# Optimization experiments

Measured on AMD Instinct MI355X. Metric: run time of the kernel, lower is better.

## Reference

```python
import jax, jax.numpy as jnp
import numpy as np

NUM_HEADS = 16
THETA = 10000.0


def _rope(x, cos, sin):
    # x: [B, H, S, d_k]; cos/sin: [S, d_k//2]
    x_even = x[..., 0::2]
    x_odd = x[..., 1::2]
    out_even = x_even * cos - x_odd * sin
    out_odd = x_odd * cos + x_even * sin
    # interleave back to original even/odd layout
    return jnp.stack([out_even, out_odd], axis=-1).reshape(x.shape)


def setup_inputs() -> dict:
    key = jax.random.key(0)
    ks = jax.random.split(key, 5)
    B, S, D = 2, 2048, 1024
    std = 2.0 / (D + D)
    return {
        "x": jax.random.normal(ks[0], (B, S, D), dtype=jnp.float32),
        "w_q": jax.random.normal(ks[1], (D, D), dtype=jnp.float32) * std,
        "w_k": jax.random.normal(ks[2], (D, D), dtype=jnp.float32) * std,
        "w_v": jax.random.normal(ks[3], (D, D), dtype=jnp.float32) * std,
        "w_o": jax.random.normal(ks[4], (D, D), dtype=jnp.float32) * std,
    }


def reference(x, w_q, w_k, w_v, w_o):
    B, S, D = x.shape
    H = NUM_HEADS
    d_k = D // H

    # QKV projections: x @ W.T
    q = jnp.einsum('bsd,ed->bse', x, w_q).reshape(B, S, H, d_k).transpose(0, 2, 1, 3)
    k = jnp.einsum('bsd,ed->bse', x, w_k).reshape(B, S, H, d_k).transpose(0, 2, 1, 3)
    v = jnp.einsum('bsd,ed->bse', x, w_v).reshape(B, S, H, d_k).transpose(0, 2, 1, 3)

    # RoPE (token_positions = arange(S))
    pos = jnp.arange(S, dtype=jnp.float32)
    inv_freq = 1.0 / (THETA ** (2.0 * jnp.arange(d_k // 2, dtype=jnp.float32) / d_k))
    angles = pos[:, None] * inv_freq[None, :]  # [S, d_k//2]
    cos, sin = jnp.cos(angles), jnp.sin(angles)
    q = _rope(q, cos, sin)
    k = _rope(k, cos, sin)

    # causal attention
    scores = jnp.einsum('bhqd,bhkd->bhqk', q, k) / jnp.sqrt(jnp.float32(d_k))
    causal = jnp.tril(jnp.ones((S, S), dtype=bool))
    scores = jnp.where(causal[None, None], scores, -jnp.inf)
    attn = jax.nn.softmax(scores, axis=-1)
    out = jnp.einsum('bhqk,bhkd->bhqd', attn, v)  # [B, H, S, d_k]

    out = out.transpose(0, 2, 1, 3).reshape(B, S, D)
    return jnp.einsum('bsd,ed->bse', out, w_o)
```

## Files before the change

### kernel.cpp

```cpp
#include <hip/hip_runtime.h>

typedef unsigned short u16;
typedef unsigned int u32;
typedef short bf16x8 __attribute__((ext_vector_type(8)));
typedef float f32x4 __attribute__((ext_vector_type(4)));

#define CSC 0.18033688011112042f

__device__ __forceinline__ u16 f2bf(float f) {
    union { float f; unsigned u; } x; x.f = f;
    unsigned r = x.u + 0x7fffu + ((x.u >> 16) & 1u);
    return (u16)(r >> 16);
}
__device__ __forceinline__ float bf2f(u16 v) {
    union { unsigned u; float f; } x; x.u = ((unsigned)v) << 16;
    return x.f;
}
__device__ __forceinline__ float exp2_fast(float x) {
#if __has_builtin(__builtin_amdgcn_exp2f)
    return __builtin_amdgcn_exp2f(x);
#else
    return exp2f(x);
#endif
}
__device__ __forceinline__ void gl_lds16(const u16* g, u16* l) {
#if __has_builtin(__builtin_amdgcn_global_load_lds)
    __builtin_amdgcn_global_load_lds(
        (const __attribute__((address_space(1))) unsigned int*)g,
        (__attribute__((address_space(3))) unsigned int*)l, 16, 0, 0);
#else
    *(bf16x8*)l = *(const bf16x8*)g;
#endif
}
__device__ __forceinline__ int ileave(int x) {
    return (x < 16) ? (x << 1) : (((x - 16) << 1) | 1);
}

__global__ void cvt_all_kernel(const float* __restrict__ x, const float* __restrict__ wq,
                               const float* __restrict__ wk, const float* __restrict__ wv,
                               const float* __restrict__ wo,
                               u16* __restrict__ xb, u16* __restrict__ qkvw,
                               u16* __restrict__ ow) {
    int i = blockIdx.x * 256 + threadIdx.x;
    const float4* src;
    ushort4* dst;
    if (i < 1048576) {
        src = (const float4*)x + i;
        dst = (ushort4*)xb + i;
    } else {
        int r = i - 1048576;
        int m = r >> 18;
        int off = r & 262143;
        const float* s4 = (m == 0) ? wq : (m == 1) ? wk : (m == 2) ? wv : wo;
        u16* d = (m < 3) ? (qkvw + (size_t)m * 1048576) : ow;
        src = (const float4*)s4 + off;
        dst = (ushort4*)d + off;
    }
    float4 v = *src;
    ushort4 o;
    o.x = f2bf(v.x); o.y = f2bf(v.y); o.z = f2bf(v.z); o.w = f2bf(v.w);
    *dst = o;
}

__global__ void rope_kernel(u16* __restrict__ qb, u16* __restrict__ kb) {
    int idx = blockIdx.x * 256 + threadIdx.x;
    u16* buf;
    float scale;
    if (blockIdx.y == 0) { buf = qb; scale = CSC; } else { buf = kb; scale = 1.0f; }
    int g   = idx & 7;
    int row = idx >> 3;
    int s   = row & 2047;
    u16* p = buf + (size_t)row * 64 + g * 8;
    bf16x8 v = *(bf16x8*)p;
    bf16x8 o;
    #pragma unroll
    for (int q = 0; q < 4; ++q) {
        int i = g * 4 + q;
        float inv = exp2_fast((float)i * -0.4152410118609203f);
        float ang = (float)s * inv;
        float sn, cs;
        sincosf(ang, &sn, &cs);
        float e  = bf2f(((u16*)&v)[2 * q]);
        float od = bf2f(((u16*)&v)[2 * q + 1]);
        ((u16*)&o)[2 * q]     = f2bf((e * cs - od * sn) * scale);
        ((u16*)&o)[2 * q + 1] = f2bf((od * cs + e * sn) * scale);
    }
    *(bf16x8*)p = o;
}

__global__ __launch_bounds__(256) void gemm_qkv(const u16* __restrict__ A,
                                                const u16* __restrict__ Bw,
                                                u16* __restrict__ C, int K) {
    __shared__ __align__(16) u16 SH[8448];
    u16* As = SH;
    u16* Bs = SH + 4096;
    const int tid  = threadIdx.x;
    const int bm   = blockIdx.x * 128;
    const int bn   = blockIdx.y * 128;
    const int wave = tid >> 6, lane = tid & 63;
    const int wm   = (wave >> 1) * 64, wn = (wave & 1) * 64;
    const int l16  = lane & 15, quad = lane >> 4;
    const int mat  = bn >> 10;

    f32x4 acc[4][4];
    #pragma unroll
    for (int i = 0; i < 4; i++)
        #pragma unroll
        for (int j = 0; j < 4; j++)
            #pragma unroll
            for (int e = 0; e < 4; e++) acc[i][j][e] = 0.0f;

    const int srow = tid >> 2, scol = (tid & 3) * 8;
    const u16* gA0 = A  + (size_t)(bm + srow) * K + scol;
    const u16* gA1 = A  + (size_t)(bm + 64 + srow) * K + scol;
    const u16* gB0 = Bw + (size_t)(bn + srow) * K + scol;
    const u16* gB1 = Bw + (size_t)(bn + 64 + srow) * K + scol;
    u16* lA0 = &As[(size_t)tid * 8];
    u16* lA1 = &As[(size_t)(tid + 256) * 8];
    u16* lB0 = &Bs[(size_t)tid * 8];
    u16* lB1 = &Bs[(size_t)(tid + 256) * 8];

    for (int k0 = 0; k0 < K; k0 += 32) {
        __syncthreads();
        gl_lds16(gA0 + k0, lA0);
        gl_lds16(gA1 + k0, lA1);
        gl_lds16(gB0 + k0, lB0);
        gl_lds16(gB1 + k0, lB1);
        __syncthreads();
        bf16x8 af[4], bfr[4];
        #pragma unroll
        for (int i = 0; i < 4; i++) af[i]  = *(const bf16x8*)&As[(wm + i * 16 + l16) * 32 + quad * 8];
        #pragma unroll
        for (int j = 0; j < 4; j++) bfr[j] = *(const bf16x8*)&Bs[(wn + j * 16 + l16) * 32 + quad * 8];
        #pragma unroll
        for (int i = 0; i < 4; i++)
            #pragma unroll
            for (int j = 0; j < 4; j++)
                acc[i][j] = __builtin_amdgcn_mfma_f32_16x16x32_bf16(af[i], bfr[j], acc[i][j], 0, 0, 0);
    }

    const int b  = bm >> 11, sb = bm & 2047;
    if (mat < 2) {
        #pragma unroll
        for (int pass = 0; pass < 2; ++pass) {
            __syncthreads();
            if ((wn >> 6) == pass) {
                #pragma unroll
                for (int i = 0; i < 4; i++)
                    #pragma unroll
                    for (int j = 0; j < 4; j++)
                        #pragma unroll
                        for (int r = 0; r < 4; r++) {
                            int rl = wm + i * 16 + quad * 4 + r;
                            int cl = j * 16 + l16;
                            SH[rl * 66 + cl] = f2bf(acc[i][j][r]);
                        }
            }
            __syncthreads();
            int rl   = tid >> 1;
            int half = (tid & 1) * 32;
            int c    = (bn + pass * 64) & 1023;
            int h    = c >> 6;
            int s    = sb + rl;
            u16* dst = C + (size_t)mat * 4194304 +
                       (((size_t)(b * 16 + h) * 2048 + s) * 64) + half;
            const u16* srcp = &SH[rl * 66 + half];
            #pragma unroll
            for (int kk = 0; kk < 4; ++kk)
                *(bf16x8*)(dst + kk * 8) = *(const bf16x8*)(srcp + kk * 8);
        }
    } else {
        #pragma unroll
        for (int pass = 0; pass < 2; ++pass) {
            __syncthreads();
            if ((wn >> 6) == pass) {
                #pragma unroll
                for (int i = 0; i < 4; i++)
                    #pragma unroll
                    for (int j = 0; j < 4; j++)
                        #pragma unroll
                        for (int r = 0; r < 4; r++) {
                            int row = j * 16 + l16;
                            int ml  = wm + i * 16 + quad * 4 + r;
                            int sp  = (ml & ~31) | ileave(ml & 31);
                            SH[row * 130 + sp] = f2bf(acc[i][j][r]);
                        }
            }
            __syncthreads();
            int row = tid >> 2, seg = tid & 3;
            int cc  = (bn + pass * 64 + row) & 1023;
            int h = cc >> 6, dv = cc & 63;
            u16* dst = C + (size_t)8388608 +
                       (((size_t)(b * 16 + h) * 64 + dv) * 2048) + sb + seg * 32;
            const u16* srcp = &SH[row * 130 + seg * 32];
            #pragma unroll
            for (int kk = 0; kk < 4; ++kk)
                *(bf16x8*)(dst + kk * 8) = *(const bf16x8*)(srcp + kk * 8);
        }
    }
}

__global__ __launch_bounds__(256, 2) void gemm_out(const u16* __restrict__ A,
                                                   const u16* __restrict__ Bw,
                                                   float* __restrict__ C, int K) {
    __shared__ __align__(16) u16 As[128 * 32];
    __shared__ __align__(16) u16 Bs[64 * 32];
    const int tid  = threadIdx.x;
    const int bm   = blockIdx.x * 128;
    const int bn   = blockIdx.y * 64;
    const int wave = tid >> 6, lane = tid & 63;
    const int wm   = wave * 32;
    const int l16  = lane & 15, quad = lane >> 4;

    f32x4 acc[2][4];
    #pragma unroll
    for (int i = 0; i < 2; i++)
        #pragma unroll
        for (int j = 0; j < 4; j++)
            #pragma unroll
            for (int e = 0; e < 4; e++) acc[i][j][e] = 0.0f;

    const int srow = tid >> 2, scol = (tid & 3) * 8;
    const u16* gA0 = A  + (size_t)(bm + srow) * K + scol;
    const u16* gA1 = A  + (size_t)(bm + 64 + srow) * K + scol;
    const u16* gB0 = Bw + (size_t)(bn + srow) * K + scol;
    u16* lA0 = &As[(size_t)tid * 8];
    u16* lA1 = &As[(size_t)(tid + 256) * 8];
    u16* lB0 = &Bs[(size_t)tid * 8];

    for (int k0 = 0; k0 < K; k0 += 32) {
        __syncthreads();
        gl_lds16(gA0 + k0, lA0);
        gl_lds16(gA1 + k0, lA1);
        gl_lds16(gB0 + k0, lB0);
        __syncthreads();
        bf16x8 af[2], bfr[4];
        #pragma unroll
        for (int i = 0; i < 2; i++) af[i]  = *(const bf16x8*)&As[(wm + i * 16 + l16) * 32 + quad * 8];
        #pragma unroll
        for (int j = 0; j < 4; j++) bfr[j] = *(const bf16x8*)&Bs[(j * 16 + l16) * 32 + quad * 8];
        #pragma unroll
        for (int i = 0; i < 2; i++)
            #pragma unroll
            for (int j = 0; j < 4; j++)
                acc[i][j] = __builtin_amdgcn_mfma_f32_16x16x32_bf16(af[i], bfr[j], acc[i][j], 0, 0, 0);
    }

    #pragma unroll
    for (int i = 0; i < 2; i++)
        #pragma unroll
        for (int j = 0; j < 4; j++)
            #pragma unroll
            for (int r = 0; r < 4; r++) {
                int mr = bm + wm + i * 16 + quad * 4 + r;
                int nc = bn + j * 16 + l16;
                C[(size_t)mr * 1024 + nc] = acc[i][j][r];
            }
}

__global__ __launch_bounds__(256, 2) void attn_kernel(const u16* __restrict__ Q,
                                                      const u16* __restrict__ Kb,
                                                      const u16* __restrict__ Vt,
                                                      u16* __restrict__ Oout) {
    __shared__ __align__(16) u16 KV[2][8192];
    __shared__ __align__(16) u16 PW[4 * 1152];
    const int tid  = threadIdx.x;
    const int wave = tid >> 6, lane = tid & 63;
    const int l16  = lane & 15, quad = lane >> 4;
    const int bid  = blockIdx.x;
    const int j    = (bid >> 3) & 15;
    const int bh   = (bid & 7) * 4 + (bid >> 7);
    const int T    = 32 - j;
    const int qA0  = j * 64 + wave * 16;
    const int qB0  = (31 - j) * 64 + wave * 16;

    const u16* Qh = Q  + (size_t)bh * 2048 * 64;
    const u16* Kh = Kb + (size_t)bh * 2048 * 64;
    const u16* Vh = Vt + (size_t)bh * 64 * 2048;

    bf16x8 qAf0 = *(const bf16x8*)&Qh[(size_t)(qA0 + l16) * 64 + quad * 8];
    bf16x8 qAf1 = *(const bf16x8*)&Qh[(size_t)(qA0 + l16) * 64 + 32 + quad * 8];
    bf16x8 qBf0 = *(const bf16x8*)&Qh[(size_t)(qB0 + l16) * 64 + quad * 8];
    bf16x8 qBf1 = *(const bf16x8*)&Qh[(size_t)(qB0 + l16) * 64 + 32 + quad * 8];

    f32x4 oA[4], oB[4];
    float lsA[4], lsB[4];
    #pragma unroll
    for (int t = 0; t < 4; t++)
        #pragma unroll
        for (int e = 0; e < 4; e++) { oA[t][e] = 0.0f; oB[t][e] = 0.0f; }
    #pragma unroll
    for (int r = 0; r < 4; r++) { lsA[r] = 0.0f; lsB[r] = 0.0f; }

    const u16* gK = Kh + (size_t)(tid >> 2) * 64 + (tid & 3) * 8;
    const u16* gV = Vh + (size_t)(tid >> 2) * 2048 + (tid & 3) * 8;

    u16* pw16 = PW + wave * 1152;
    u32* pw32 = (u32*)pw16;

    auto stage = [&](int t, int buf) {
        u16* base = KV[buf];
        gl_lds16(gK + (size_t)t * 4096,      base + (size_t)tid * 8);
        gl_lds16(gK + (size_t)t * 4096 + 32, base + 2048 + (size_t)tid * 8);
        gl_lds16(gV + (size_t)t * 64,        base + 4096 + (size_t)tid * 8);
        gl_lds16(gV + (size_t)t * 64 + 32,   base + 6144 + (size_t)tid * 8);
    };

    auto side = [&](const bf16x8& q0f, const bf16x8& q1f, bf16x8* kf0, bf16x8* kf1,
                    bf16x8* vf0, bf16x8* vf1, f32x4* o, float* ls,
                    int q0, int kbase, bool diag) {
        f32x4 s[4];
        #pragma unroll
        for (int n = 0; n < 4; n++) {
            #pragma unroll
            for (int e = 0; e < 4; e++) s[n][e] = 0.0f;
            s[n] = __builtin_amdgcn_mfma_f32_16x16x32_bf16(q0f, kf0[n], s[n], 0, 0, 0);
            s[n] = __builtin_amdgcn_mfma_f32_16x16x32_bf16(q1f, kf1[n], s[n], 0, 0, 0);
        }
        float p[4][4];
        #pragma unroll
        for (int n = 0; n < 4; n++)
            #pragma unroll
            for (int r = 0; r < 4; r++) {
                float v = exp2_fast(s[n][r]);
                if (diag) {
                    int row = q0 + quad * 4 + r;
                    v = (kbase + n * 16 + l16 > row) ? 0.0f : v;
                }
                p[n][r] = v;
                ls[r] += v;
            }
        #pragma unroll
        for (int c = 0; c < 2; c++)
            #pragma unroll
            for (int r = 0; r < 4; r++)
                pw32[(quad * 4 + r) * 36 + c * 16 + l16] =
                    (u32)f2bf(p[2 * c][r]) | ((u32)f2bf(p[2 * c + 1][r]) << 16);
        asm volatile("s_waitcnt lgkmcnt(0)" ::: "memory");
        bf16x8 pf0 = *(const bf16x8*)&pw16[l16 * 72 + quad * 8];
        bf16x8 pf1 = *(const bf16x8*)&pw16[l16 * 72 + 32 + quad * 8];
        #pragma unroll
        for (int dn = 0; dn < 4; dn++) {
            o[dn] = __builtin_amdgcn_mfma_f32_16x16x32_bf16(pf0, vf0[dn], o[dn], 0, 0, 0);
            o[dn] = __builtin_amdgcn_mfma_f32_16x16x32_bf16(pf1, vf1[dn], o[dn], 0, 0, 0);
        }
    };

    stage(0, 0);
    for (int t = 0; t < T; ++t) {
        __syncthreads();
        if (t + 1 < T) stage(t + 1, (t + 1) & 1);
        const u16* B = KV[t & 1];
        bf16x8 kf0[4], kf1[4], vf0[4], vf1[4];
        #pragma unroll
        for (int n = 0; n < 4; n++) {
            int ri = (n * 16 + l16) * 32 + quad * 8;
            kf0[n] = *(const bf16x8*)&B[ri];
            kf1[n] = *(const bf16x8*)&B[2048 + ri];
            vf0[n] = *(const bf16x8*)&B[4096 + ri];
            vf1[n] = *(const bf16x8*)&B[6144 + ri];
        }
        const int kbase = t * 64;
        side(qBf0, qBf1, kf0, kf1, vf0, vf1, oB, lsB, qB0, kbase, t == T - 1);
        if (t <= j)
            side(qAf0, qAf1, kf0, kf1, vf0, vf1, oA, lsA, qA0, kbase, t == j);
    }

    #pragma unroll
    for (int off = 1; off < 16; off <<= 1)
        #pragma unroll
        for (int r = 0; r < 4; r++) {
            lsA[r] += __shfl_xor(lsA[r], off);
            lsB[r] += __shfl_xor(lsB[r], off);
        }

    const int b = bh >> 4, h = bh & 15;
    #pragma unroll
    for (int r = 0; r < 4; r++) {
        float iA = 1.0f / lsA[r];
        float iB = 1.0f / lsB[r];
        int sA = qA0 + quad * 4 + r;
        int sB = qB0 + quad * 4 + r;
        #pragma unroll
        for (int dn = 0; dn < 4; dn++) {
            int d = h * 64 + dn * 16 + l16;
            Oout[((size_t)b * 2048 + sA) * 1024 + d] = f2bf(oA[dn][r] * iA);
            Oout[((size_t)b * 2048 + sB) * 1024 + d] = f2bf(oB[dn][r] * iB);
        }
    }
}

extern "C" void kernel_launch(void* const* d_in, const int* in_sizes, int n_in,
                              void* d_out, int out_size, void* d_ws, size_t ws_size,
                              hipStream_t stream) {
    const float* x  = (const float*)d_in[0];
    const float* wq = (const float*)d_in[1];
    const float* wk = (const float*)d_in[2];
    const float* wv = (const float*)d_in[3];
    const float* wo = (const float*)d_in[4];
    float* out = (float*)d_out;

    const int M = 4096, D = 1024;
    u16* xb    = (u16*)d_ws;
    u16* qkvw  = xb   + (size_t)M * D;
    u16* ow    = qkvw + (size_t)3 * D * D;
    u16* qkv   = ow   + (size_t)D * D;
    u16* qb    = qkv;
    u16* kb    = qkv + (size_t)M * D;
    u16* vtb   = qkv + (size_t)2 * M * D;
    u16* aob   = qkv + (size_t)3 * M * D;

    cvt_all_kernel<<<8192, 256, 0, stream>>>(x, wq, wk, wv, wo, xb, qkvw, ow);

    dim3 gq(32, 24);
    gemm_qkv<<<gq, 256, 0, stream>>>(xb, qkvw, qkv, D);

    dim3 gr(2048, 2);
    rope_kernel<<<gr, 256, 0, stream>>>(qb, kb);

    attn_kernel<<<512, 256, 0, stream>>>(qb, kb, vtb, aob);

    dim3 go(32, 16);
    gemm_out<<<go, 256, 0, stream>>>(aob, ow, out, D);
}
```

Before: 198.9 us.

## Fuse RoPE into QKV GEMM epilogue, retile attention and output GEMM

The standalone RoPE kernel is removed. A cos/sin table is now computed in the prep kernel and RoPE plus the Q scale are applied in the QKV GEMM epilogue, which saves one read-write pass over Q and K and one launch. The attention kernel drops the paired-tile scheme in favour of one query tile per block, with 1024 blocks, occupancy raised to 4, V fragments read directly from global memory and only K staged in LDS. The output GEMM's K step is widened to 64 to halve the number of barriers. The new attention layout risks load imbalance across blocks and higher V load latency from the uncached global reads.

```diff
diff --git a/kernel.cpp b/kernel.cpp
--- a/kernel.cpp
+++ b/kernel.cpp
@@ -36,12 +36,22 @@
     return (x < 16) ? (x << 1) : (((x - 16) << 1) | 1);
 }
 
-__global__ void cvt_all_kernel(const float* __restrict__ x, const float* __restrict__ wq,
-                               const float* __restrict__ wk, const float* __restrict__ wv,
-                               const float* __restrict__ wo,
-                               u16* __restrict__ xb, u16* __restrict__ qkvw,
-                               u16* __restrict__ ow) {
+__global__ void prep_kernel(const float* __restrict__ x, const float* __restrict__ wq,
+                            const float* __restrict__ wk, const float* __restrict__ wv,
+                            const float* __restrict__ wo,
+                            u16* __restrict__ xb, u16* __restrict__ qkvw,
+                            u16* __restrict__ ow, float2* __restrict__ tab) {
     int i = blockIdx.x * 256 + threadIdx.x;
+    if (i >= 2097152) {
+        int e  = i - 2097152;
+        int s  = e >> 5, ii = e & 31;
+        float inv = exp2_fast((float)ii * -0.4152410118609203f);
+        float ang = (float)s * inv;
+        float sn, cs;
+        sincosf(ang, &sn, &cs);
+        tab[e] = make_float2(cs, sn);
+        return;
+    }
     const float4* src;
     ushort4* dst;
     if (i < 1048576) {
@@ -62,35 +72,10 @@
     *dst = o;
 }
 
-__global__ void rope_kernel(u16* __restrict__ qb, u16* __restrict__ kb) {
-    int idx = blockIdx.x * 256 + threadIdx.x;
-    u16* buf;
-    float scale;
-    if (blockIdx.y == 0) { buf = qb; scale = CSC; } else { buf = kb; scale = 1.0f; }
-    int g   = idx & 7;
-    int row = idx >> 3;
-    int s   = row & 2047;
-    u16* p = buf + (size_t)row * 64 + g * 8;
-    bf16x8 v = *(bf16x8*)p;
-    bf16x8 o;
-    #pragma unroll
-    for (int q = 0; q < 4; ++q) {
-        int i = g * 4 + q;
-        float inv = exp2_fast((float)i * -0.4152410118609203f);
-        float ang = (float)s * inv;
-        float sn, cs;
-        sincosf(ang, &sn, &cs);
-        float e  = bf2f(((u16*)&v)[2 * q]);
-        float od = bf2f(((u16*)&v)[2 * q + 1]);
-        ((u16*)&o)[2 * q]     = f2bf((e * cs - od * sn) * scale);
-        ((u16*)&o)[2 * q + 1] = f2bf((od * cs + e * sn) * scale);
-    }
-    *(bf16x8*)p = o;
-}
-
 __global__ __launch_bounds__(256) void gemm_qkv(const u16* __restrict__ A,
                                                 const u16* __restrict__ Bw,
-                                                u16* __restrict__ C, int K) {
+                                                u16* __restrict__ C,
+                                                const float2* __restrict__ tab, int K) {
     __shared__ __align__(16) u16 SH[8448];
     u16* As = SH;
     u16* Bs = SH + 4096;
@@ -141,6 +126,7 @@
 
     const int b  = bm >> 11, sb = bm & 2047;
     if (mat < 2) {
+        const float scale = (mat == 0) ? CSC : 1.0f;
         #pragma unroll
         for (int pass = 0; pass < 2; ++pass) {
             __syncthreads();
@@ -164,10 +150,22 @@
             int s    = sb + rl;
             u16* dst = C + (size_t)mat * 4194304 +
                        (((size_t)(b * 16 + h) * 2048 + s) * 64) + half;
-            const u16* srcp = &SH[rl * 66 + half];
-            #pragma unroll
-            for (int kk = 0; kk < 4; ++kk)
-                *(bf16x8*)(dst + kk * 8) = *(const bf16x8*)(srcp + kk * 8);
+            const float2* trow = tab + (size_t)s * 32;
+            #pragma unroll
+            for (int kk = 0; kk < 4; ++kk) {
+                bf16x8 ch = *(const bf16x8*)&SH[rl * 66 + half + kk * 8];
+                int p0 = (half + kk * 8) >> 1;
+                bf16x8 oc;
+                #pragma unroll
+                for (int pi = 0; pi < 4; ++pi) {
+                    float2 t = trow[p0 + pi];
+                    float e  = bf2f(((const u16*)&ch)[2 * pi]);
+                    float od = bf2f(((const u16*)&ch)[2 * pi + 1]);
+                    ((u16*)&oc)[2 * pi]     = f2bf((e * t.x - od * t.y) * scale);
+                    ((u16*)&oc)[2 * pi + 1] = f2bf((od * t.x + e * t.y) * scale);
+                }
+                *(bf16x8*)(dst + kk * 8) = oc;
+            }
         }
     } else {
         #pragma unroll
@@ -203,8 +201,8 @@
 __global__ __launch_bounds__(256, 2) void gemm_out(const u16* __restrict__ A,
                                                    const u16* __restrict__ Bw,
                                                    float* __restrict__ C, int K) {
-    __shared__ __align__(16) u16 As[128 * 32];
-    __shared__ __align__(16) u16 Bs[64 * 32];
+    __shared__ __align__(16) u16 As[128 * 64];
+    __shared__ __align__(16) u16 Bs[64 * 64];
     const int tid  = threadIdx.x;
     const int bm   = blockIdx.x * 128;
     const int bn   = blockIdx.y * 64;
@@ -220,30 +218,34 @@
             #pragma unroll
             for (int e = 0; e < 4; e++) acc[i][j][e] = 0.0f;
 
-    const int srow = tid >> 2, scol = (tid & 3) * 8;
-    const u16* gA0 = A  + (size_t)(bm + srow) * K + scol;
-    const u16* gA1 = A  + (size_t)(bm + 64 + srow) * K + scol;
-    const u16* gB0 = Bw + (size_t)(bn + srow) * K + scol;
-    u16* lA0 = &As[(size_t)tid * 8];
-    u16* lA1 = &As[(size_t)(tid + 256) * 8];
-    u16* lB0 = &Bs[(size_t)tid * 8];
-
-    for (int k0 = 0; k0 < K; k0 += 32) {
+    const int srow = tid >> 3, scol = (tid & 7) * 8;
+    const u16* gA = A  + (size_t)(bm + srow) * K + scol;
+    const u16* gB = Bw + (size_t)(bn + srow) * K + scol;
+
+    for (int k0 = 0; k0 < K; k0 += 64) {
         __syncthreads();
-        gl_lds16(gA0 + k0, lA0);
-        gl_lds16(gA1 + k0, lA1);
-        gl_lds16(gB0 + k0, lB0);
+        gl_lds16(gA + k0,          &As[(size_t)tid * 8]);
+        gl_lds16(gA + 32 * K + k0, &As[(size_t)(tid + 256) * 8]);
+        gl_lds16(gA + 64 * K + k0, &As[(size_t)(tid + 512) * 8]);
+        gl_lds16(gA + 96 * K + k0, &As[(size_t)(tid + 768) * 8]);
+        gl_lds16(gB + k0,          &Bs[(size_t)tid * 8]);
+        gl_lds16(gB + 32 * K + k0, &Bs[(size_t)(tid + 256) * 8]);
         __syncthreads();
-        bf16x8 af[2], bfr[4];
-        #pragma unroll
-        for (int i = 0; i < 2; i++) af[i]  = *(const bf16x8*)&As[(wm + i * 16 + l16) * 32 + quad * 8];
-        #pragma unroll
-        for (int j = 0; j < 4; j++) bfr[j] = *(const bf16x8*)&Bs[(j * 16 + l16) * 32 + quad * 8];
-        #pragma unroll
-        for (int i = 0; i < 2; i++)
+        #pragma unroll
+        for (int hh = 0; hh < 2; ++hh) {
+            bf16x8 af[2], bfr[4];
+            #pragma unroll
+            for (int i = 0; i < 2; i++)
+                af[i]  = *(const bf16x8*)&As[(wm + i * 16 + l16) * 64 + hh * 32 + quad * 8];
             #pragma unroll
             for (int j = 0; j < 4; j++)
-                acc[i][j] = __builtin_amdgcn_mfma_f32_16x16x32_bf16(af[i], bfr[j], acc[i][j], 0, 0, 0);
+                bfr[j] = *(const bf16x8*)&Bs[(j * 16 + l16) * 64 + hh * 32 + quad * 8];
+            #pragma unroll
+            for (int i = 0; i < 2; i++)
+                #pragma unroll
+                for (int j = 0; j < 4; j++)
+                    acc[i][j] = __builtin_amdgcn_mfma_f32_16x16x32_bf16(af[i], bfr[j], acc[i][j], 0, 0, 0);
+        }
     }
 
     #pragma unroll
@@ -258,65 +260,74 @@
             }
 }
 
-__global__ __launch_bounds__(256, 2) void attn_kernel(const u16* __restrict__ Q,
+__global__ __launch_bounds__(256, 4) void attn_kernel(const u16* __restrict__ Q,
                                                       const u16* __restrict__ Kb,
                                                       const u16* __restrict__ Vt,
                                                       u16* __restrict__ Oout) {
-    __shared__ __align__(16) u16 KV[2][8192];
-    __shared__ __align__(16) u16 PW[4 * 1152];
+    __shared__ __align__(16) u16 Ks[2][4096];
+    __shared__ __align__(16) u16 PW[4][1152];
     const int tid  = threadIdx.x;
     const int wave = tid >> 6, lane = tid & 63;
     const int l16  = lane & 15, quad = lane >> 4;
     const int bid  = blockIdx.x;
-    const int j    = (bid >> 3) & 15;
-    const int bh   = (bid & 7) * 4 + (bid >> 7);
-    const int T    = 32 - j;
-    const int qA0  = j * 64 + wave * 16;
-    const int qB0  = (31 - j) * 64 + wave * 16;
+    const int c    = bid & 7;
+    const int m    = bid >> 3;
+    const int bh   = (m & 3) * 8 + c;
+    const int qt   = 31 - (m >> 2);
+    const int T    = qt + 1;
+    const int q0   = qt * 64 + wave * 16;
 
     const u16* Qh = Q  + (size_t)bh * 2048 * 64;
     const u16* Kh = Kb + (size_t)bh * 2048 * 64;
     const u16* Vh = Vt + (size_t)bh * 64 * 2048;
 
-    bf16x8 qAf0 = *(const bf16x8*)&Qh[(size_t)(qA0 + l16) * 64 + quad * 8];
-    bf16x8 qAf1 = *(const bf16x8*)&Qh[(size_t)(qA0 + l16) * 64 + 32 + quad * 8];
-    bf16x8 qBf0 = *(const bf16x8*)&Qh[(size_t)(qB0 + l16) * 64 + quad * 8];
-    bf16x8 qBf1 = *(const bf16x8*)&Qh[(size_t)(qB0 + l16) * 64 + 32 + quad * 8];
-
-    f32x4 oA[4], oB[4];
-    float lsA[4], lsB[4];
+    bf16x8 qf0 = *(const bf16x8*)&Qh[(size_t)(q0 + l16) * 64 + quad * 8];
+    bf16x8 qf1 = *(const bf16x8*)&Qh[(size_t)(q0 + l16) * 64 + 32 + quad * 8];
+
+    f32x4 o[4];
+    float ls[4];
     #pragma unroll
     for (int t = 0; t < 4; t++)
         #pragma unroll
-        for (int e = 0; e < 4; e++) { oA[t][e] = 0.0f; oB[t][e] = 0.0f; }
-    #pragma unroll
-    for (int r = 0; r < 4; r++) { lsA[r] = 0.0f; lsB[r] = 0.0f; }
-
-    const u16* gK = Kh + (size_t)(tid >> 2) * 64 + (tid & 3) * 8;
-    const u16* gV = Vh + (size_t)(tid >> 2) * 2048 + (tid & 3) * 8;
-
-    u16* pw16 = PW + wave * 1152;
+        for (int e = 0; e < 4; e++) o[t][e] = 0.0f;
+    #pragma unroll
+    for (int r = 0; r < 4; r++) ls[r] = 0.0f;
+
+    const u16* gK = Kh + (size_t)(tid >> 3) * 64 + (tid & 7) * 8;
+    u16* pw16 = PW[wave];
     u32* pw32 = (u32*)pw16;
 
     auto stage = [&](int t, int buf) {
-        u16* base = KV[buf];
-        gl_lds16(gK + (size_t)t * 4096,      base + (size_t)tid * 8);
-        gl_lds16(gK + (size_t)t * 4096 + 32, base + 2048 + (size_t)tid * 8);
-        gl_lds16(gV + (size_t)t * 64,        base + 4096 + (size_t)tid * 8);
-        gl_lds16(gV + (size_t)t * 64 + 32,   base + 6144 + (size_t)tid * 8);
+        gl_lds16(gK + (size_t)t * 4096,        &Ks[buf][(size_t)tid * 8]);
+        gl_lds16(gK + (size_t)t * 4096 + 2048, &Ks[buf][(size_t)(tid + 256) * 8]);
     };
 
-    auto side = [&](const bf16x8& q0f, const bf16x8& q1f, bf16x8* kf0, bf16x8* kf1,
-                    bf16x8* vf0, bf16x8* vf1, f32x4* o, float* ls,
-                    int q0, int kbase, bool diag) {
+    stage(0, 0);
+    for (int t = 0; t < T; ++t) {
+        __syncthreads();
+        if (t + 1 < T) stage(t + 1, (t + 1) & 1);
+        const int kbase = t * 64;
+
+        bf16x8 vf0[4], vf1[4];
+        #pragma unroll
+        for (int n = 0; n < 4; n++) {
+            vf0[n] = *(const bf16x8*)&Vh[(size_t)(n * 16 + l16) * 2048 + kbase + quad * 8];
+            vf1[n] = *(const bf16x8*)&Vh[(size_t)(n * 16 + l16) * 2048 + kbase + 32 + quad * 8];
+        }
+
+        const u16* B = Ks[t & 1];
         f32x4 s[4];
         #pragma unroll
         for (int n = 0; n < 4; n++) {
+            bf16x8 kf0 = *(const bf16x8*)&B[(n * 16 + l16) * 64 + quad * 8];
+            bf16x8 kf1 = *(const bf16x8*)&B[(n * 16 + l16) * 64 + 32 + quad * 8];
             #pragma unroll
             for (int e = 0; e < 4; e++) s[n][e] = 0.0f;
-            s[n] = __builtin_amdgcn_mfma_f32_16x16x32_bf16(q0f, kf0[n], s[n], 0, 0, 0);
-            s[n] = __builtin_amdgcn_mfma_f32_16x16x32_bf16(q1f, kf1[n], s[n], 0, 0, 0);
-        }
+            s[n] = __builtin_amdgcn_mfma_f32_16x16x32_bf16(qf0, kf0, s[n], 0, 0, 0);
+            s[n] = __builtin_amdgcn_mfma_f32_16x16x32_bf16(qf1, kf1, s[n], 0, 0, 0);
+        }
+
+        const bool diag = (t == T - 1);
         float p[4][4];
         #pragma unroll
         for (int n = 0; n < 4; n++)
@@ -331,11 +342,11 @@
                 ls[r] += v;
             }
         #pragma unroll
-        for (int c = 0; c < 2; c++)
+        for (int cc = 0; cc < 2; cc++)
             #pragma unroll
             for (int r = 0; r < 4; r++)
-                pw32[(quad * 4 + r) * 36 + c * 16 + l16] =
-                    (u32)f2bf(p[2 * c][r]) | ((u32)f2bf(p[2 * c + 1][r]) << 16);
+                pw32[(quad * 4 + r) * 36 + cc * 16 + l16] =
+                    (u32)f2bf(p[2 * cc][r]) | ((u32)f2bf(p[2 * cc + 1][r]) << 16);
         asm volatile("s_waitcnt lgkmcnt(0)" ::: "memory");
         bf16x8 pf0 = *(const bf16x8*)&pw16[l16 * 72 + quad * 8];
         bf16x8 pf1 = *(const bf16x8*)&pw16[l16 * 72 + 32 + quad * 8];
@@ -344,48 +355,22 @@
             o[dn] = __builtin_amdgcn_mfma_f32_16x16x32_bf16(pf0, vf0[dn], o[dn], 0, 0, 0);
             o[dn] = __builtin_amdgcn_mfma_f32_16x16x32_bf16(pf1, vf1[dn], o[dn], 0, 0, 0);
         }
-    };
-
-    stage(0, 0);
-    for (int t = 0; t < T; ++t) {
-        __syncthreads();
-        if (t + 1 < T) stage(t + 1, (t + 1) & 1);
-        const u16* B = KV[t & 1];
-        bf16x8 kf0[4], kf1[4], vf0[4], vf1[4];
-        #pragma unroll
-        for (int n = 0; n < 4; n++) {
-            int ri = (n * 16 + l16) * 32 + quad * 8;
-            kf0[n] = *(const bf16x8*)&B[ri];
-            kf1[n] = *(const bf16x8*)&B[2048 + ri];
-            vf0[n] = *(const bf16x8*)&B[4096 + ri];
-            vf1[n] = *(const bf16x8*)&B[6144 + ri];
-        }
-        const int kbase = t * 64;
-        side(qBf0, qBf1, kf0, kf1, vf0, vf1, oB, lsB, qB0, kbase, t == T - 1);
-        if (t <= j)
-            side(qAf0, qAf1, kf0, kf1, vf0, vf1, oA, lsA, qA0, kbase, t == j);
     }
 
     #pragma unroll
     for (int off = 1; off < 16; off <<= 1)
         #pragma unroll
-        for (int r = 0; r < 4; r++) {
-            lsA[r] += __shfl_xor(lsA[r], off);
-            lsB[r] += __shfl_xor(lsB[r], off);
-        }
+        for (int r = 0; r < 4; r++) ls[r] += __shfl_xor(ls[r], off);
 
     const int b = bh >> 4, h = bh & 15;
     #pragma unroll
     for (int r = 0; r < 4; r++) {
-        float iA = 1.0f / lsA[r];
-        float iB = 1.0f / lsB[r];
-        int sA = qA0 + quad * 4 + r;
-        int sB = qB0 + quad * 4 + r;
+        float inv = 1.0f / ls[r];
+        int s = q0 + quad * 4 + r;
         #pragma unroll
         for (int dn = 0; dn < 4; dn++) {
             int d = h * 64 + dn * 16 + l16;
-            Oout[((size_t)b * 2048 + sA) * 1024 + d] = f2bf(oA[dn][r] * iA);
-            Oout[((size_t)b * 2048 + sB) * 1024 + d] = f2bf(oB[dn][r] * iB);
+            Oout[((size_t)b * 2048 + s) * 1024 + d] = f2bf(o[dn][r] * inv);
         }
     }
 }
@@ -409,16 +394,14 @@
     u16* kb    = qkv + (size_t)M * D;
     u16* vtb   = qkv + (size_t)2 * M * D;
     u16* aob   = qkv + (size_t)3 * M * D;
-
-    cvt_all_kernel<<<8192, 256, 0, stream>>>(x, wq, wk, wv, wo, xb, qkvw, ow);
+    float2* tab = (float2*)(aob + (size_t)M * D);
+
+    prep_kernel<<<8448, 256, 0, stream>>>(x, wq, wk, wv, wo, xb, qkvw, ow, tab);
 
     dim3 gq(32, 24);
-    gemm_qkv<<<gq, 256, 0, stream>>>(xb, qkvw, qkv, D);
-
-    dim3 gr(2048, 2);
-    rope_kernel<<<gr, 256, 0, stream>>>(qb, kb);
-
-    attn_kernel<<<512, 256, 0, stream>>>(qb, kb, vtb, aob);
+    gemm_qkv<<<gq, 256, 0, stream>>>(xb, qkvw, qkv, tab, D);
+
+    attn_kernel<<<1024, 256, 0, stream>>>(qb, kb, vtb, aob);
 
     dim3 go(32, 16);
     gemm_out<<<go, 256, 0, stream>>>(aob, ow, out, D);
```

After: 241.6 us. 21.5% more time.
